# Kernel tuning notes

Measured on AMD Instinct MI355X. Metric: run time of the kernel, lower is better.

The kernel has to match this reference:

```python
import jax, jax.numpy as jnp
import numpy as np

DECAY = 0.99
EPS = 1e-05


def setup_inputs() -> dict:
    key = jax.random.key(0)
    k1, k2, k3 = jax.random.split(key, 3)
    return {
        "input": jax.random.normal(k1, (32, 64, 64, 64), dtype=jnp.float32),
        "embed": jax.random.normal(k2, (64, 512), dtype=jnp.float32),
        "cluster_size": jnp.zeros((512,), dtype=jnp.float32),
        "embed_avg": jax.random.normal(k3, (64, 512), dtype=jnp.float32),
    }


def reference(input, embed, cluster_size, embed_avg):
    n_embed = embed.shape[1]
    flatten = input.reshape(-1, input.shape[-1])  # [N, dim]
    dist = (
        jnp.sum(flatten * flatten, axis=1, keepdims=True)
        - 2.0 * flatten @ embed
        + jnp.sum(embed * embed, axis=0, keepdims=True)
    )  # [N, n_embed]
    embed_ind_flat = jnp.argmin(dist, axis=1)  # [N]
    embed_ind = embed_ind_flat.reshape(input.shape[:-1])
    quantize = jnp.take(embed.T, embed_ind_flat, axis=0).reshape(input.shape)
    diff = jnp.mean((quantize - input) ** 2)

    # EMA codebook update (training path; buffer updates returned as outputs)
    embed_onehot_sum = jnp.zeros((n_embed,), dtype=flatten.dtype).at[embed_ind_flat].add(1.0)
    embed_sum = jax.ops.segment_sum(flatten, embed_ind_flat, num_segments=n_embed).T  # [dim, n_embed]
    new_cluster_size = cluster_size * DECAY + (1.0 - DECAY) * embed_onehot_sum
    new_embed_avg = embed_avg * DECAY + (1.0 - DECAY) * embed_sum
    n = jnp.sum(new_cluster_size)
    cs = (new_cluster_size + EPS) / (n + n_embed * EPS) * n
    new_embed = new_embed_avg / cs[None, :]

    # straight-through estimator
    quantize_st = input + jax.lax.stop_gradient(quantize - input)
    return (quantize_st, diff, embed_ind, new_embed, new_cluster_size, new_embed_avg)
```

## Files before the change

kernel.cpp:

```cpp
#include <hip/hip_runtime.h>

#define DIM     64
#define N_EMBED 512
#define N_ROWS  131072
#define XPAD    132

__global__ void se_kernel(const float* __restrict__ embed, float* __restrict__ se) {
    int j = blockIdx.x * blockDim.x + threadIdx.x;
    if (j >= N_EMBED) return;
    float s = 0.f;
#pragma unroll
    for (int d = 0; d < DIM; ++d) {
        float e = embed[d * N_EMBED + j];
        s = fmaf(e, e, s);
    }
    se[j] = s;
}

__launch_bounds__(256, 2)
__global__ void vq_assign(const float* __restrict__ input,
                          const float* __restrict__ embed,
                          const float* __restrict__ se,
                          float* __restrict__ out_ind,
                          int*   __restrict__ ind) {
    __shared__ float Xs[64][XPAD];
    __shared__ float Es[64][XPAD];
    __shared__ float sxs[128];

    const int t    = threadIdx.x;
    const int row0 = blockIdx.x * 128;
    const int tr   = t >> 4;
    const int tc   = t & 15;

#pragma unroll
    for (int ph = 0; ph < 8; ++ph) {
        int idx = ph * 256 + t;
        int row = idx >> 4;
        int kq  = idx & 15;
        float4 v = *reinterpret_cast<const float4*>(
            &input[(size_t)(row0 + row) * 64 + kq * 4]);
        Xs[kq * 4 + 0][row] = v.x;
        Xs[kq * 4 + 1][row] = v.y;
        Xs[kq * 4 + 2][row] = v.z;
        Xs[kq * 4 + 3][row] = v.w;
    }
    __syncthreads();

    if (t < 128) {
        float s = 0.f;
#pragma unroll 8
        for (int k = 0; k < 64; ++k) { float x = Xs[k][t]; s = fmaf(x, x, s); }
        sxs[t] = s;
    }

    float bestd[8], sx[8];
    int   bestj[8];
#pragma unroll
    for (int r = 0; r < 8; ++r) { bestd[r] = INFINITY; bestj[r] = 0; }

    for (int chunk = 0; chunk < 4; ++chunk) {
        const int ccb = chunk * 128;
        __syncthreads();
#pragma unroll
        for (int ph = 0; ph < 8; ++ph) {
            int idx = ph * 256 + t;
            int k   = idx >> 5;
            int cq  = idx & 31;
            float4 v = *reinterpret_cast<const float4*>(
                &embed[k * N_EMBED + ccb + cq * 4]);
            *reinterpret_cast<float4*>(&Es[k][cq * 4]) = v;
        }
        __syncthreads();
        if (chunk == 0) {
#pragma unroll
            for (int r = 0; r < 8; ++r) sx[r] = sxs[tr * 8 + r];
        }

        float acc[8][8];
#pragma unroll
        for (int r = 0; r < 8; ++r)
#pragma unroll
            for (int c = 0; c < 8; ++c) acc[r][c] = 0.f;

#pragma unroll 2
        for (int k = 0; k < 64; ++k) {
            float a[8], b[8];
            *reinterpret_cast<float4*>(&a[0]) = *reinterpret_cast<const float4*>(&Xs[k][tr * 8]);
            *reinterpret_cast<float4*>(&a[4]) = *reinterpret_cast<const float4*>(&Xs[k][tr * 8 + 4]);
            *reinterpret_cast<float4*>(&b[0]) = *reinterpret_cast<const float4*>(&Es[k][tc * 8]);
            *reinterpret_cast<float4*>(&b[4]) = *reinterpret_cast<const float4*>(&Es[k][tc * 8 + 4]);
#pragma unroll
            for (int r = 0; r < 8; ++r)
#pragma unroll
                for (int c = 0; c < 8; ++c)
                    acc[r][c] = fmaf(a[r], b[c], acc[r][c]);
        }

#pragma unroll
        for (int c = 0; c < 8; ++c) {
            int j = ccb + tc * 8 + c;
            float sej = se[j];
#pragma unroll
            for (int r = 0; r < 8; ++r) {
                float d = (sx[r] - 2.f * acc[r][c]) + sej;
                if (d < bestd[r]) { bestd[r] = d; bestj[r] = j; }
            }
        }
    }

    __syncthreads();
    float* rd = &Es[0][0];
    int*   rj = (int*)(rd + 128 * 17);
#pragma unroll
    for (int r = 0; r < 8; ++r) {
        rd[(tr * 8 + r) * 17 + tc] = bestd[r];
        rj[(tr * 8 + r) * 17 + tc] = bestj[r];
    }
    __syncthreads();
    if (t < 128) {
        float bd = rd[t * 17 + 0];
        int   bj = rj[t * 17 + 0];
#pragma unroll
        for (int w = 1; w < 16; ++w) {
            float dw = rd[t * 17 + w];
            int   jw = rj[t * 17 + w];
            if (dw < bd || (dw == bd && jw < bj)) { bd = dw; bj = jw; }
        }
        out_ind[row0 + t] = (float)bj;
        ind[row0 + t]     = bj;
    }
}

__launch_bounds__(256, 1)
__global__ void vq_post(const float* __restrict__ input,
                        const float* __restrict__ embed,
                        const int* __restrict__ ind,
                        float* __restrict__ out_q,
                        float* __restrict__ esum,
                        float* __restrict__ counts,
                        double* __restrict__ diff_acc) {
    __shared__ float lesum[DIM * N_EMBED];
    __shared__ float lcount[N_EMBED];
    __shared__ float wsum[4];
    const int t = threadIdx.x;

    float4* l4 = reinterpret_cast<float4*>(lesum);
#pragma unroll
    for (int i = 0; i < 32; ++i) l4[t + i * 256] = float4{0.f, 0.f, 0.f, 0.f};
    lcount[t] = 0.f;
    lcount[t + 256] = 0.f;
    __syncthreads();

    float dsum = 0.f;
#pragma unroll
    for (int rr = 0; rr < 2; ++rr) {
        const int row = blockIdx.x * 512 + rr * 256 + t;
        const int j = ind[row];
        atomicAdd(&lcount[j], 1.0f);
        const float* rp = input + (size_t)row * DIM;
        float* oq = out_q + (size_t)row * DIM;
#pragma unroll
        for (int d = 0; d < DIM; d += 4) {
            float4 v = *reinterpret_cast<const float4*>(rp + d);
            float q0 = embed[(d + 0) * N_EMBED + j];
            float q1 = embed[(d + 1) * N_EMBED + j];
            float q2 = embed[(d + 2) * N_EMBED + j];
            float q3 = embed[(d + 3) * N_EMBED + j];
            float t0 = q0 - v.x;
            float t1 = q1 - v.y;
            float t2 = q2 - v.z;
            float t3 = q3 - v.w;
            float4 o;
            o.x = v.x + t0; o.y = v.y + t1; o.z = v.z + t2; o.w = v.w + t3;
            *reinterpret_cast<float4*>(oq + d) = o;
            dsum = fmaf(t0, t0, dsum);
            dsum = fmaf(t1, t1, dsum);
            dsum = fmaf(t2, t2, dsum);
            dsum = fmaf(t3, t3, dsum);
            atomicAdd(&lesum[(d + 0) * N_EMBED + j], v.x);
            atomicAdd(&lesum[(d + 1) * N_EMBED + j], v.y);
            atomicAdd(&lesum[(d + 2) * N_EMBED + j], v.z);
            atomicAdd(&lesum[(d + 3) * N_EMBED + j], v.w);
        }
    }
    __syncthreads();

    for (int i = t; i < DIM * N_EMBED; i += 256) {
        float v = lesum[i];
        if (v != 0.f) atomicAdd(&esum[i], v);
    }
    for (int c = t; c < N_EMBED; c += 256) {
        float v = lcount[c];
        if (v != 0.f) atomicAdd(&counts[c], v);
    }

    for (int off = 32; off > 0; off >>= 1) dsum += __shfl_down(dsum, off, 64);
    int lane = t & 63, wid = t >> 6;
    if (lane == 0) wsum[wid] = dsum;
    __syncthreads();
    if (t == 0) {
        float b = wsum[0] + wsum[1] + wsum[2] + wsum[3];
        atomicAdd(diff_acc, (double)b);
    }
}

__global__ void vq_finalize(const float* __restrict__ cluster_size,
                            const float* __restrict__ embed_avg,
                            const float* __restrict__ counts,
                            const float* __restrict__ esum,
                            const double* __restrict__ diff_acc,
                            float* __restrict__ out_diff,
                            float* __restrict__ out_new_embed,
                            float* __restrict__ out_ncs,
                            float* __restrict__ out_nea) {
    int t = threadIdx.x;
    const float DEC = 0.99f, OMD = 0.01f, EPSF = 1e-5f;

    float ncs = cluster_size[t] * DEC + OMD * counts[t];
    out_ncs[t] = ncs;

    __shared__ float red[512];
    red[t] = ncs;
    __syncthreads();
    for (int s = 256; s > 0; s >>= 1) {
        if (t < s) red[t] += red[t + s];
        __syncthreads();
    }
    float n = red[0];
    float cs = (ncs + EPSF) / (n + 512.0f * EPSF) * n;

#pragma unroll
    for (int d = 0; d < DIM; ++d) {
        float es = embed_avg[d * N_EMBED + t] * DEC + OMD * esum[d * N_EMBED + t];
        out_nea[d * N_EMBED + t] = es;
        out_new_embed[d * N_EMBED + t] = es / cs;
    }
    if (t == 0) out_diff[0] = (float)(*diff_acc * (1.0 / 8388608.0));
}

extern "C" void kernel_launch(void* const* d_in, const int* in_sizes, int n_in,
                              void* d_out, int out_size, void* d_ws, size_t ws_size,
                              hipStream_t stream) {
    const float* input        = (const float*)d_in[0];
    const float* embed        = (const float*)d_in[1];
    const float* cluster_size = (const float*)d_in[2];
    const float* embed_avg    = (const float*)d_in[3];

    float* out_q    = (float*)d_out;
    float* out_diff = out_q + 8388608;
    float* out_ind  = out_diff + 1;
    float* out_ne   = out_ind + 131072;
    float* out_ncs  = out_ne + 32768;
    float* out_nea  = out_ncs + 512;

    char*   ws       = (char*)d_ws;
    double* diff_acc = (double*)ws;
    float*  counts   = (float*)(ws + 256);
    float*  se       = (float*)(ws + 4096);
    int*    ind      = (int*)(ws + 8192);
    float*  esum     = (float*)(ws + 8192 + 524288);

    hipMemsetAsync(ws, 0, 4096, stream);
    hipMemsetAsync(ws + 8192 + 524288, 0, 131072, stream);
    se_kernel<<<2, 256, 0, stream>>>(embed, se);
    vq_assign<<<1024, 256, 0, stream>>>(input, embed, se, out_ind, ind);
    vq_post<<<256, 256, 0, stream>>>(input, embed, ind, out_q, esum, counts, diff_acc);
    vq_finalize<<<1, 512, 0, stream>>>(cluster_size, embed_avg, counts, esum, diff_acc,
                                       out_diff, out_ne, out_ncs, out_nea);
}
```

Measured before the change: 286.3 us.

## Transpose codebook for gathers, swizzle LDS, widen post kernel, split finalize

The prep kernel now also writes a row-major transposed copy of the codebook, so vq_post can fetch each row's code vector with contiguous float4 loads instead of 64 strided scalar loads. The shared-memory layout of the codebook tile in vq_assign gets an XOR swizzle to reduce LDS bank conflicts on the b-operand reads. vq_post moves to 512 threads, one row per thread. The single-block finalize is split into a reduction kernel plus a 64-block elementwise kernel so the embed update runs in parallel. These add an extra launch and extra workspace, and the transposed path falls back when the workspace is too small.

```diff
diff --git a/kernel.cpp b/kernel.cpp
--- a/kernel.cpp
+++ b/kernel.cpp
@@ -5,14 +5,25 @@
 #define N_ROWS  131072
 #define XPAD    132
 
-__global__ void se_kernel(const float* __restrict__ embed, float* __restrict__ se) {
+__global__ void prep_kernel(const float* __restrict__ embed,
+                            float* __restrict__ se,
+                            float* __restrict__ embed_t,
+                            int do_et) {
     int j = blockIdx.x * blockDim.x + threadIdx.x;
     if (j >= N_EMBED) return;
     float s = 0.f;
 #pragma unroll
-    for (int d = 0; d < DIM; ++d) {
-        float e = embed[d * N_EMBED + j];
-        s = fmaf(e, e, s);
+    for (int d = 0; d < DIM; d += 4) {
+        float b0 = embed[(d + 0) * N_EMBED + j];
+        float b1 = embed[(d + 1) * N_EMBED + j];
+        float b2 = embed[(d + 2) * N_EMBED + j];
+        float b3 = embed[(d + 3) * N_EMBED + j];
+        s = fmaf(b0, b0, s); s = fmaf(b1, b1, s);
+        s = fmaf(b2, b2, s); s = fmaf(b3, b3, s);
+        if (do_et) {
+            float4 v; v.x = b0; v.y = b1; v.z = b2; v.w = b3;
+            *reinterpret_cast<float4*>(&embed_t[j * DIM + d]) = v;
+        }
     }
     se[j] = s;
 }
@@ -31,6 +42,7 @@
     const int row0 = blockIdx.x * 128;
     const int tr   = t >> 4;
     const int tc   = t & 15;
+    const int bx   = ((tc >> 2) & 1) * 4;
 
 #pragma unroll
     for (int ph = 0; ph < 8; ++ph) {
@@ -68,7 +80,7 @@
             int cq  = idx & 31;
             float4 v = *reinterpret_cast<const float4*>(
                 &embed[k * N_EMBED + ccb + cq * 4]);
-            *reinterpret_cast<float4*>(&Es[k][cq * 4]) = v;
+            *reinterpret_cast<float4*>(&Es[k][(cq * 4) ^ (((cq >> 3) & 1) * 4)]) = v;
         }
         __syncthreads();
         if (chunk == 0) {
@@ -87,8 +99,8 @@
             float a[8], b[8];
             *reinterpret_cast<float4*>(&a[0]) = *reinterpret_cast<const float4*>(&Xs[k][tr * 8]);
             *reinterpret_cast<float4*>(&a[4]) = *reinterpret_cast<const float4*>(&Xs[k][tr * 8 + 4]);
-            *reinterpret_cast<float4*>(&b[0]) = *reinterpret_cast<const float4*>(&Es[k][tc * 8]);
-            *reinterpret_cast<float4*>(&b[4]) = *reinterpret_cast<const float4*>(&Es[k][tc * 8 + 4]);
+            *reinterpret_cast<float4*>(&b[0]) = *reinterpret_cast<const float4*>(&Es[k][(tc * 8) ^ bx]);
+            *reinterpret_cast<float4*>(&b[4]) = *reinterpret_cast<const float4*>(&Es[k][(tc * 8 + 4) ^ bx]);
 #pragma unroll
             for (int r = 0; r < 8; ++r)
 #pragma unroll
@@ -131,34 +143,52 @@
     }
 }
 
-__launch_bounds__(256, 1)
+__launch_bounds__(512, 1)
 __global__ void vq_post(const float* __restrict__ input,
                         const float* __restrict__ embed,
+                        const float* __restrict__ embed_t,
                         const int* __restrict__ ind,
                         float* __restrict__ out_q,
                         float* __restrict__ esum,
                         float* __restrict__ counts,
-                        double* __restrict__ diff_acc) {
+                        double* __restrict__ diff_acc,
+                        int have_et) {
     __shared__ float lesum[DIM * N_EMBED];
     __shared__ float lcount[N_EMBED];
-    __shared__ float wsum[4];
+    __shared__ float wsum[8];
     const int t = threadIdx.x;
 
     float4* l4 = reinterpret_cast<float4*>(lesum);
 #pragma unroll
-    for (int i = 0; i < 32; ++i) l4[t + i * 256] = float4{0.f, 0.f, 0.f, 0.f};
+    for (int i = 0; i < 16; ++i) l4[t + i * 512] = float4{0.f, 0.f, 0.f, 0.f};
     lcount[t] = 0.f;
-    lcount[t + 256] = 0.f;
-    __syncthreads();
-
+    __syncthreads();
+
+    const int row = blockIdx.x * 512 + t;
+    const int j = ind[row];
+    atomicAdd(&lcount[j], 1.0f);
+    const float* rp = input + (size_t)row * DIM;
+    float* oq = out_q + (size_t)row * DIM;
     float dsum = 0.f;
-#pragma unroll
-    for (int rr = 0; rr < 2; ++rr) {
-        const int row = blockIdx.x * 512 + rr * 256 + t;
-        const int j = ind[row];
-        atomicAdd(&lcount[j], 1.0f);
-        const float* rp = input + (size_t)row * DIM;
-        float* oq = out_q + (size_t)row * DIM;
+
+    if (have_et) {
+        const float* qp = embed_t + (size_t)j * DIM;
+#pragma unroll
+        for (int d = 0; d < DIM; d += 4) {
+            float4 v = *reinterpret_cast<const float4*>(rp + d);
+            float4 q = *reinterpret_cast<const float4*>(qp + d);
+            float t0 = q.x - v.x, t1 = q.y - v.y, t2 = q.z - v.z, t3 = q.w - v.w;
+            float4 o;
+            o.x = v.x + t0; o.y = v.y + t1; o.z = v.z + t2; o.w = v.w + t3;
+            *reinterpret_cast<float4*>(oq + d) = o;
+            dsum = fmaf(t0, t0, dsum); dsum = fmaf(t1, t1, dsum);
+            dsum = fmaf(t2, t2, dsum); dsum = fmaf(t3, t3, dsum);
+            atomicAdd(&lesum[(d + 0) * N_EMBED + j], v.x);
+            atomicAdd(&lesum[(d + 1) * N_EMBED + j], v.y);
+            atomicAdd(&lesum[(d + 2) * N_EMBED + j], v.z);
+            atomicAdd(&lesum[(d + 3) * N_EMBED + j], v.w);
+        }
+    } else {
 #pragma unroll
         for (int d = 0; d < DIM; d += 4) {
             float4 v = *reinterpret_cast<const float4*>(rp + d);
@@ -166,17 +196,12 @@
             float q1 = embed[(d + 1) * N_EMBED + j];
             float q2 = embed[(d + 2) * N_EMBED + j];
             float q3 = embed[(d + 3) * N_EMBED + j];
-            float t0 = q0 - v.x;
-            float t1 = q1 - v.y;
-            float t2 = q2 - v.z;
-            float t3 = q3 - v.w;
+            float t0 = q0 - v.x, t1 = q1 - v.y, t2 = q2 - v.z, t3 = q3 - v.w;
             float4 o;
             o.x = v.x + t0; o.y = v.y + t1; o.z = v.z + t2; o.w = v.w + t3;
             *reinterpret_cast<float4*>(oq + d) = o;
-            dsum = fmaf(t0, t0, dsum);
-            dsum = fmaf(t1, t1, dsum);
-            dsum = fmaf(t2, t2, dsum);
-            dsum = fmaf(t3, t3, dsum);
+            dsum = fmaf(t0, t0, dsum); dsum = fmaf(t1, t1, dsum);
+            dsum = fmaf(t2, t2, dsum); dsum = fmaf(t3, t3, dsum);
             atomicAdd(&lesum[(d + 0) * N_EMBED + j], v.x);
             atomicAdd(&lesum[(d + 1) * N_EMBED + j], v.y);
             atomicAdd(&lesum[(d + 2) * N_EMBED + j], v.z);
@@ -185,13 +210,13 @@
     }
     __syncthreads();
 
-    for (int i = t; i < DIM * N_EMBED; i += 256) {
+    for (int i = t; i < DIM * N_EMBED; i += 512) {
         float v = lesum[i];
         if (v != 0.f) atomicAdd(&esum[i], v);
     }
-    for (int c = t; c < N_EMBED; c += 256) {
-        float v = lcount[c];
-        if (v != 0.f) atomicAdd(&counts[c], v);
+    {
+        float v = lcount[t];
+        if (v != 0.f) atomicAdd(&counts[t], v);
     }
 
     for (int off = 32; off > 0; off >>= 1) dsum += __shfl_down(dsum, off, 64);
@@ -199,26 +224,20 @@
     if (lane == 0) wsum[wid] = dsum;
     __syncthreads();
     if (t == 0) {
-        float b = wsum[0] + wsum[1] + wsum[2] + wsum[3];
+        float b = 0.f;
+#pragma unroll
+        for (int w = 0; w < 8; ++w) b += wsum[w];
         atomicAdd(diff_acc, (double)b);
     }
 }
 
-__global__ void vq_finalize(const float* __restrict__ cluster_size,
-                            const float* __restrict__ embed_avg,
-                            const float* __restrict__ counts,
-                            const float* __restrict__ esum,
-                            const double* __restrict__ diff_acc,
-                            float* __restrict__ out_diff,
-                            float* __restrict__ out_new_embed,
-                            float* __restrict__ out_ncs,
-                            float* __restrict__ out_nea) {
+__global__ void fin_a(const float* __restrict__ cluster_size,
+                      const float* __restrict__ counts,
+                      float* __restrict__ out_ncs,
+                      float* __restrict__ nstore) {
     int t = threadIdx.x;
-    const float DEC = 0.99f, OMD = 0.01f, EPSF = 1e-5f;
-
-    float ncs = cluster_size[t] * DEC + OMD * counts[t];
+    float ncs = cluster_size[t] * 0.99f + 0.01f * counts[t];
     out_ncs[t] = ncs;
-
     __shared__ float red[512];
     red[t] = ncs;
     __syncthreads();
@@ -226,16 +245,27 @@
         if (t < s) red[t] += red[t + s];
         __syncthreads();
     }
-    float n = red[0];
+    if (t == 0) nstore[0] = red[0];
+}
+
+__global__ void fin_b(const float* __restrict__ embed_avg,
+                      const float* __restrict__ esum,
+                      const float* __restrict__ out_ncs,
+                      const float* __restrict__ nstore,
+                      const double* __restrict__ diff_acc,
+                      float* __restrict__ out_ne,
+                      float* __restrict__ out_nea,
+                      float* __restrict__ out_diff) {
+    int e = blockIdx.x * 512 + threadIdx.x;
+    const float EPSF = 1e-5f;
+    float n = nstore[0];
+    int j = e & (N_EMBED - 1);
+    float ncs = out_ncs[j];
     float cs = (ncs + EPSF) / (n + 512.0f * EPSF) * n;
-
-#pragma unroll
-    for (int d = 0; d < DIM; ++d) {
-        float es = embed_avg[d * N_EMBED + t] * DEC + OMD * esum[d * N_EMBED + t];
-        out_nea[d * N_EMBED + t] = es;
-        out_new_embed[d * N_EMBED + t] = es / cs;
-    }
-    if (t == 0) out_diff[0] = (float)(*diff_acc * (1.0 / 8388608.0));
+    float es = embed_avg[e] * 0.99f + 0.01f * esum[e];
+    out_nea[e] = es;
+    out_ne[e] = es / cs;
+    if (e == 0) out_diff[0] = (float)(*diff_acc * (1.0 / 8388608.0));
 }
 
 extern "C" void kernel_launch(void* const* d_in, const int* in_sizes, int n_in,
@@ -255,16 +285,23 @@
 
     char*   ws       = (char*)d_ws;
     double* diff_acc = (double*)ws;
+    float*  nstore   = (float*)(ws + 64);
     float*  counts   = (float*)(ws + 256);
     float*  se       = (float*)(ws + 4096);
     int*    ind      = (int*)(ws + 8192);
     float*  esum     = (float*)(ws + 8192 + 524288);
+    float*  embed_t  = (float*)(ws + 8192 + 524288 + 131072);
+
+    const size_t need_et = 8192 + 524288 + 131072 + 131072;
+    const int have_et = (ws_size >= need_et) ? 1 : 0;
 
     hipMemsetAsync(ws, 0, 4096, stream);
     hipMemsetAsync(ws + 8192 + 524288, 0, 131072, stream);
-    se_kernel<<<2, 256, 0, stream>>>(embed, se);
+    prep_kernel<<<2, 256, 0, stream>>>(embed, se, embed_t, have_et);
     vq_assign<<<1024, 256, 0, stream>>>(input, embed, se, out_ind, ind);
-    vq_post<<<256, 256, 0, stream>>>(input, embed, ind, out_q, esum, counts, diff_acc);
-    vq_finalize<<<1, 512, 0, stream>>>(cluster_size, embed_avg, counts, esum, diff_acc,
-                                       out_diff, out_ne, out_ncs, out_nea);
-}
+    vq_post<<<256, 512, 0, stream>>>(input, embed, embed_t, ind, out_q, esum, counts,
+                                     diff_acc, have_et);
+    fin_a<<<1, 512, 0, stream>>>(cluster_size, counts, out_ncs, nstore);
+    fin_b<<<64, 512, 0, stream>>>(embed_avg, esum, out_ncs, nstore, diff_acc,
+                                  out_ne, out_nea, out_diff);
+}
```

Result: faster. 280.7 us (-2.0%).
